# Kernel optimization log

Measured on AMD Instinct MI355X. Metric: run time of the kernel, lower is better.

## Reference

```python
import jax, jax.numpy as jnp
import numpy as np

NUM_GROUPS = 32
EPS = 1e-6


def group_norm(x, gamma, beta):
    # x: [B, C, H, W]; GroupNorm over (channels-in-group, H, W)
    B, C, H, W = x.shape
    xg = x.reshape(B, NUM_GROUPS, C // NUM_GROUPS, H, W)
    mean = xg.mean(axis=(2, 3, 4), keepdims=True)
    var = xg.var(axis=(2, 3, 4), keepdims=True)
    xn = ((xg - mean) * jax.lax.rsqrt(var + EPS)).reshape(B, C, H, W)
    return xn * gamma[None, :, None, None] + beta[None, :, None, None]


def conv1x1(x, w, b):
    # 1x1 conv == channel-mixing matmul. w: [C_out, C_in]
    return jnp.einsum('bchw,oc->bohw', x, w) + b[None, :, None, None]


def setup_inputs() -> dict:
    key = jax.random.key(0)
    ks = jax.random.split(key, 6)
    B, C, H, W = 8, 256, 64, 64
    s = 1.0 / np.sqrt(C)  # fan-in scaled weights (like Conv2d default)
    inp = {
        'x': jax.random.normal(ks[0], (B, C, H, W), jnp.float32),
        'gamma': jnp.ones((C,), jnp.float32),
        'beta': jnp.zeros((C,), jnp.float32),
        'wq': jax.random.normal(ks[1], (C, C), jnp.float32) * s,
        'bq': jnp.zeros((C,), jnp.float32),
        'wk': jax.random.normal(ks[2], (C, C), jnp.float32) * s,
        'bk': jnp.zeros((C,), jnp.float32),
        'wv': jax.random.normal(ks[3], (C, C), jnp.float32) * s,
        'bv': jnp.zeros((C,), jnp.float32),
        'wo': jax.random.normal(ks[4], (C, C), jnp.float32) * s,
        'bo': jnp.zeros((C,), jnp.float32),
    }
    return inp


def reference(x, gamma, beta, wq, bq, wk, bk, wv, bv, wo, bo):
    B, C, H, W = x.shape
    h = group_norm(x, gamma, beta)
    q = conv1x1(h, wq, bq)
    k = conv1x1(h, wk, bk)
    v = conv1x1(h, wv, bv)
    # elu + 1 feature map (nonnegative kernel features)
    q = jax.nn.elu(q) + 1.0
    k = jax.nn.elu(k) + 1.0
    N = H * W
    kf = k.reshape(B, C, N)            # [B, C, N]
    vf = v.reshape(B, C, N)            # [B, C, N]
    qf = q.reshape(B, C, N)            # [B, C, N]
    # kv = k @ v^T : [B, C, C]
    kv = jnp.einsum('bcn,bdn->bcd', kf, vf)
    # h_out[b, n, d] = sum_c q[b, c, n] * kv[b, c, d]; stored channel-first
    h_out = jnp.einsum('bcn,bcd->bdn', qf, kv).reshape(B, C, H, W)
    return x + conv1x1(h_out, wo, bo)
```

## Files before the change

kernel.cpp:

```cpp
#include <hip/hip_runtime.h>
#include <math.h>

#define C_DIM 256
#define N_DIM 4096
#define B_DIM 8

typedef __attribute__((ext_vector_type(8))) short bf16x8;
typedef __attribute__((ext_vector_type(4))) float f32x4;
typedef __attribute__((ext_vector_type(8))) unsigned short us8;
typedef __attribute__((ext_vector_type(4))) unsigned short us4;

__device__ inline unsigned short f2bf(float f) {
    unsigned int u = __float_as_uint(f);
    u += 0x7fffu + ((u >> 16) & 1u);
    return (unsigned short)(u >> 16);
}

__device__ inline void gload_lds16(const void* g, void* l) {
    __builtin_amdgcn_global_load_lds(
        (const __attribute__((address_space(1))) unsigned int*)g,
        (__attribute__((address_space(3))) unsigned int*)l, 16, 0, 0);
}

__global__ __launch_bounds__(256) void prep_kernel(
    const float* __restrict__ wq, const float* __restrict__ wk,
    const float* __restrict__ wv, const float* __restrict__ wo,
    const float* __restrict__ bk, const float* __restrict__ bv,
    const float* __restrict__ x,
    unsigned short* __restrict__ wqb, unsigned short* __restrict__ wkvb,
    unsigned short* __restrict__ wob, float* __restrict__ bkv,
    float2* __restrict__ sums)
{
    int z = blockIdx.x;
    int t = threadIdx.x;
    if (z < 256) {
        const float* s; unsigned short* d;
        int which = z >> 6;
        if (which == 0)      { s = wq; d = wqb; }
        else if (which == 1) { s = wk; d = wkvb; }
        else if (which == 2) { s = wv; d = wkvb + 65536; }
        else                 { s = wo; d = wob; }
        int idx = (z & 63) * 1024 + t * 4;
        float4 v = *(const float4*)(s + idx);
        us4 r; r[0] = f2bf(v.x); r[1] = f2bf(v.y); r[2] = f2bf(v.z); r[3] = f2bf(v.w);
        *(us4*)(d + idx) = r;
    } else if (z == 256) {
        bkv[t]       = bk[t];
        bkv[t + 256] = bv[t];
    } else {
        int bc = z - 257;
        const float* xc = x + (size_t)bc * N_DIM;
        float s = 0.f, q = 0.f;
        for (int i = t; i < 1024; i += 256) {
            float4 v = ((const float4*)xc)[i];
            s += v.x + v.y + v.z + v.w;
            q += v.x*v.x + v.y*v.y + v.z*v.z + v.w*v.w;
        }
        #pragma unroll
        for (int off = 32; off > 0; off >>= 1) {
            s += __shfl_down(s, off);
            q += __shfl_down(q, off);
        }
        __shared__ float red[8];
        int w = t >> 6;
        if ((t & 63) == 0) { red[w*2] = s; red[w*2+1] = q; }
        __syncthreads();
        if (t == 0) {
            sums[bc] = make_float2(red[0]+red[2]+red[4]+red[6],
                                   red[1]+red[3]+red[5]+red[7]);
        }
    }
}

__global__ __launch_bounds__(256) void gn_apply(const float* __restrict__ x,
                                                const float2* __restrict__ sums,
                                                const float* __restrict__ gamma,
                                                const float* __restrict__ beta,
                                                unsigned short* __restrict__ hT) {
    int b = blockIdx.y, n0 = blockIdx.x * 64;
    int t = threadIdx.x;
    __shared__ float scale[256], shift[256];
    __shared__ unsigned short trans[64][264];

    {
        int c = t;
        int gbase = c & ~7;
        float s = 0.f, q = 0.f;
        #pragma unroll
        for (int j = 0; j < 8; j++) {
            float2 u = sums[b*256 + gbase + j];
            s += u.x; q += u.y;
        }
        float mean = s * (1.f/32768.f);
        float var  = q * (1.f/32768.f) - mean*mean;
        float inv  = rsqrtf(var + 1e-6f);
        float gm = gamma[c] * inv;
        scale[c] = gm;
        shift[c] = beta[c] - mean * gm;
    }
    __syncthreads();

    #pragma unroll
    for (int it = 0; it < 16; it++) {
        int c  = it*16 + (t >> 4);
        int nl = (t & 15) * 4;
        float4 v = *(const float4*)(x + ((size_t)(b*C_DIM + c))*N_DIM + n0 + nl);
        float sc = scale[c], sh = shift[c];
        trans[nl+0][c] = f2bf(v.x*sc + sh);
        trans[nl+1][c] = f2bf(v.y*sc + sh);
        trans[nl+2][c] = f2bf(v.z*sc + sh);
        trans[nl+3][c] = f2bf(v.w*sc + sh);
    }
    __syncthreads();

    #pragma unroll
    for (int it = 0; it < 8; it++) {
        int nl = it*8 + (t >> 5);
        int cb = (t & 31) * 8;
        us8 vv = *(us8*)&trans[nl][cb];
        *(us8*)(hT + ((size_t)b*N_DIM + n0 + nl)*C_DIM + cb) = vv;
    }
}

__global__ __launch_bounds__(256) void kvred(const float* __restrict__ src, unsigned short* __restrict__ dst) {
    int gi = (blockIdx.x * 256 + threadIdx.x) * 4;
    int b = gi >> 16, idx = gi & 65535;
    float4 a = make_float4(0.f,0.f,0.f,0.f);
    #pragma unroll
    for (int sp = 0; sp < 16; sp++) {
        float4 v = *(const float4*)(src + (((size_t)b*16 + sp) << 16) + idx);
        a.x += v.x; a.y += v.y; a.z += v.z; a.w += v.w;
    }
    us4 r; r[0] = f2bf(a.x); r[1] = f2bf(a.y); r[2] = f2bf(a.z); r[3] = f2bf(a.w);
    *(us4*)(dst + ((size_t)b << 16) + idx) = r;
}

template<int MODE>
__device__ __forceinline__ void gemm_body(
    const unsigned short* __restrict__ Ab, const unsigned short* __restrict__ Bb,
    const float* __restrict__ bias, const float* __restrict__ residb,
    void* __restrict__ Cb,
    int N, int K, int k0, int Ks, int m_blk, int n_blk, bool elu,
    char* smem)
{
    unsigned short* As = (unsigned short*)smem;
    unsigned short* Bs = As + 4096;

    int t = threadIdx.x;
    int w = t >> 6, l = t & 63;
    int wm = w >> 1, wn = w & 1;
    int l15 = l & 15, quad = l >> 4;

    int srow = w * 16 + (l >> 2);
    int skc  = (l & 3) * 8;

    f32x4 acc[4][4];
    #pragma unroll
    for (int i = 0; i < 4; i++)
        #pragma unroll
        for (int j = 0; j < 4; j++)
            #pragma unroll
            for (int r = 0; r < 4; r++) acc[i][j][r] = 0.f;

    const unsigned short* Asw = As + (wm*64 + l15)*32 + quad*8;
    const unsigned short* Bsw = Bs + (wn*64 + l15)*32 + quad*8;
    unsigned short* Asl = As + w*512 + l*8;
    unsigned short* Bsl = Bs + w*512 + l*8;

    for (int kt = k0; kt < k0 + Ks; kt += 32) {
        #pragma unroll
        for (int rep = 0; rep < 2; rep++) {
            gload_lds16(Ab + (size_t)(m_blk + rep*64 + srow) * K + kt + skc, Asl + rep*2048);
            gload_lds16(Bb + (size_t)(n_blk + rep*64 + srow) * K + kt + skc, Bsl + rep*2048);
        }
        __syncthreads();
        bf16x8 af[4], bfr[4];
        #pragma unroll
        for (int i = 0; i < 4; i++) af[i]  = *(const bf16x8*)(Asw + i*16*32);
        #pragma unroll
        for (int j = 0; j < 4; j++) bfr[j] = *(const bf16x8*)(Bsw + j*16*32);
        #pragma unroll
        for (int i = 0; i < 4; i++)
            #pragma unroll
            for (int j = 0; j < 4; j++)
                acc[i][j] = __builtin_amdgcn_mfma_f32_16x16x32_bf16(af[i], bfr[j], acc[i][j], 0, 0, 0);
        __syncthreads();
    }

    if (MODE == 0 || MODE == 1 || MODE == 4) {
        unsigned short* ep = (unsigned short*)smem;
        int row0 = wm*64 + quad*4;
        int col0 = wn*64 + l15;
        #pragma unroll
        for (int i = 0; i < 4; i++) {
            #pragma unroll
            for (int j = 0; j < 4; j++) {
                int cl = col0 + j*16;
                #pragma unroll
                for (int r = 0; r < 4; r++) {
                    int rl = row0 + i*16 + r;
                    float val = acc[i][j][r];
                    if (MODE == 0) {
                        val += bias[n_blk + cl];
                        val = val > 0.f ? val + 1.f : __expf(val);
                    } else if (MODE == 1) {
                        val += bias[m_blk + rl];
                        if (elu) val = val > 0.f ? val + 1.f : __expf(val);
                    }
                    ep[rl*136 + cl] = f2bf(val);
                }
            }
        }
        __syncthreads();
        unsigned short* Cp = (unsigned short*)Cb;
        #pragma unroll
        for (int it = 0; it < 8; it++) {
            int row = it*16 + (t >> 4);
            int col = (t & 15) * 8;
            us8 vv = *(us8*)(ep + row*136 + col);
            *(us8*)(Cp + (size_t)(m_blk + row) * N + n_blk + col) = vv;
        }
    } else {
        float* ep32 = (float*)smem;
        float* Cp = (float*)Cb;
        #pragma unroll
        for (int h = 0; h < 2; h++) {
            if (wm == h) {
                int row0 = quad*4;
                int col0 = wn*64 + l15;
                #pragma unroll
                for (int i = 0; i < 4; i++)
                    #pragma unroll
                    for (int j = 0; j < 4; j++)
                        #pragma unroll
                        for (int r = 0; r < 4; r++)
                            ep32[(row0 + i*16 + r)*140 + col0 + j*16] = acc[i][j][r];
            }
            __syncthreads();
            #pragma unroll
            for (int it = 0; it < 8; it++) {
                int rl  = it*8 + (t >> 5);
                int row = m_blk + h*64 + rl;
                int col = (t & 31) * 4;
                f32x4 vv = *(f32x4*)(ep32 + rl*140 + col);
                if (MODE == 5) {
                    float bi = bias[row];
                    float4 rv = *(const float4*)(residb + (size_t)row * N + n_blk + col);
                    vv[0] += bi + rv.x; vv[1] += bi + rv.y;
                    vv[2] += bi + rv.z; vv[3] += bi + rv.w;
                }
                *(f32x4*)(Cp + (size_t)row * N + n_blk + col) = vv;
            }
            __syncthreads();
        }
    }
}

__global__ __launch_bounds__(256) void qkv_kernel(
    const unsigned short* __restrict__ hT, const unsigned short* __restrict__ wqb,
    const unsigned short* __restrict__ wkvb,
    const float* __restrict__ bq, const float* __restrict__ bkv,
    unsigned short* __restrict__ qT, unsigned short* __restrict__ kvbuf)
{
    __shared__ __align__(16) char smem[36864];
    int z = blockIdx.x;
    if (z < 512) {
        int b = z >> 6, rem = z & 63;
        int m_blk = (rem >> 1) * 128, n_blk = (rem & 1) * 128;
        gemm_body<0>(hT + (size_t)b*1048576, wqb, bq, nullptr,
                     qT + (size_t)b*1048576,
                     256, 256, 0, 256, m_blk, n_blk, true, smem);
    } else {
        int iz = z - 512;
        int b = iz >> 7, rem = iz & 127;
        int m_blk = (rem >> 5) * 128, n_blk = (rem & 31) * 128;
        gemm_body<1>(wkvb, hT + (size_t)b*1048576, bkv, nullptr,
                     kvbuf + (size_t)b*2097152,
                     4096, 256, 0, 256, m_blk, n_blk, m_blk < 256, smem);
    }
}

template<int MODE>
__global__ __launch_bounds__(256) void gemm_nt(
    const unsigned short* __restrict__ A, const unsigned short* __restrict__ B,
    const float* __restrict__ bias, const float* __restrict__ resid,
    void* __restrict__ Cout,
    int N, int K, int splits,
    size_t sA, size_t sB, size_t sC, size_t sR, int elem4)
{
    __shared__ __align__(16) char smem[36864];
    int b  = blockIdx.z / splits;
    int sp = blockIdx.z % splits;
    int Ks = K / splits;
    size_t cbase = (MODE == 3) ? ((size_t)(b*splits + sp)) * sC : (size_t)b * sC;
    void* Cb = elem4 ? (void*)((float*)Cout + cbase) : (void*)((unsigned short*)Cout + cbase);
    gemm_body<MODE>(A + b*sA, B + b*sB, bias,
                    resid ? resid + b*sR : nullptr, Cb,
                    N, K, sp*Ks, Ks, blockIdx.y*128, blockIdx.x*128, false, smem);
}

extern "C" void kernel_launch(void* const* d_in, const int* in_sizes, int n_in,
                              void* d_out, int out_size, void* d_ws, size_t ws_size,
                              hipStream_t stream) {
    const float* x     = (const float*)d_in[0];
    const float* gamma = (const float*)d_in[1];
    const float* beta  = (const float*)d_in[2];
    const float* wq    = (const float*)d_in[3];
    const float* bq    = (const float*)d_in[4];
    const float* wk    = (const float*)d_in[5];
    const float* bk    = (const float*)d_in[6];
    const float* wv    = (const float*)d_in[7];
    const float* bv    = (const float*)d_in[8];
    const float* wo    = (const float*)d_in[9];
    const float* bo    = (const float*)d_in[10];
    float* out = (float*)d_out;

    const size_t TEN = (size_t)B_DIM * C_DIM * N_DIM;
    unsigned short* ws16  = (unsigned short*)d_ws;
    unsigned short* hT    = ws16;
    unsigned short* qT    = hT    + TEN;
    unsigned short* kvbuf = qT    + TEN;
    unsigned short* kvb   = kvbuf + 2*TEN;
    unsigned short* M2b   = kvb   + 524288;
    unsigned short* wqb   = M2b   + 524288;
    unsigned short* wkvb  = wqb   + 65536;
    unsigned short* wob   = wkvb  + 131072;
    float*          bkv   = (float*)(wob + 65536);
    float2*         sums  = (float2*)(bkv + 512);
    float*          kvf   = (float*)(sums + 2048);

    prep_kernel<<<dim3(2305), 256, 0, stream>>>(wq, wk, wv, wo, bk, bv, x,
                                                wqb, wkvb, wob, bkv, sums);
    gn_apply<<<dim3(N_DIM/64, B_DIM), 256, 0, stream>>>(x, sums, gamma, beta, hT);
    qkv_kernel<<<dim3(1536), 256, 0, stream>>>(hT, wqb, wkvb, bq, bkv, qT, kvbuf);
    gemm_nt<3><<<dim3(2, 2, B_DIM*16), 256, 0, stream>>>(
        kvbuf, kvbuf + 1048576, nullptr, nullptr, kvf,
        256, 4096, 16, 2097152, 2097152, 65536, 0, 1);
    kvred<<<dim3(512), 256, 0, stream>>>(kvf, kvb);
    gemm_nt<4><<<dim3(2, 2, B_DIM), 256, 0, stream>>>(
        wob, kvb, nullptr, nullptr, M2b,
        256, 256, 1, 0, 65536, 65536, 0, 0);
    gemm_nt<5><<<dim3(32, 2, B_DIM), 256, 0, stream>>>(
        M2b, qT, bo, x, out,
        4096, 256, 1, 65536, 1048576, 1048576, 1048576, 1);
}
```

Before: 185.9 us.

## Double-buffer LDS tiles in GEMM main loop and split bf16 epilogue by halves

The GEMM body now keeps two LDS stages and issues the global-to-LDS loads for the next K tile before running the MFMAs on the current one, so memory latency overlaps with compute. It replaces the two per-iteration __syncthreads with one explicit vmcnt wait plus barrier, and raises wave priority around the MFMA block. The bf16 epilogue is staged in two 64-row halves so the LDS footprint drops to 32KB for those modes, which may allow more blocks per CU. The cost is an extra barrier round in the epilogue and some loss of scheduling freedom from the sched_barriers.

```diff
diff --git a/kernel.cpp b/kernel.cpp
--- a/kernel.cpp
+++ b/kernel.cpp
@@ -143,8 +143,7 @@
     int N, int K, int k0, int Ks, int m_blk, int n_blk, bool elu,
     char* smem)
 {
-    unsigned short* As = (unsigned short*)smem;
-    unsigned short* Bs = As + 4096;
+    unsigned short* lds = (unsigned short*)smem;
 
     int t = threadIdx.x;
     int w = t >> 6, l = t & 63;
@@ -162,63 +161,85 @@
             #pragma unroll
             for (int r = 0; r < 4; r++) acc[i][j][r] = 0.f;
 
-    const unsigned short* Asw = As + (wm*64 + l15)*32 + quad*8;
-    const unsigned short* Bsw = Bs + (wn*64 + l15)*32 + quad*8;
-    unsigned short* Asl = As + w*512 + l*8;
-    unsigned short* Bsl = Bs + w*512 + l*8;
-
-    for (int kt = k0; kt < k0 + Ks; kt += 32) {
+    auto stage = [&](int buf, int kt) {
+        unsigned short* Asl = lds + buf*8192 + t*8;
+        unsigned short* Bsl = Asl + 4096;
         #pragma unroll
         for (int rep = 0; rep < 2; rep++) {
             gload_lds16(Ab + (size_t)(m_blk + rep*64 + srow) * K + kt + skc, Asl + rep*2048);
             gload_lds16(Bb + (size_t)(n_blk + rep*64 + srow) * K + kt + skc, Bsl + rep*2048);
         }
-        __syncthreads();
+    };
+
+    const int nt = Ks >> 5;
+
+    stage(0, k0);
+    __builtin_amdgcn_sched_barrier(0);
+    asm volatile("s_waitcnt vmcnt(0)" ::: "memory");
+    __builtin_amdgcn_s_barrier();
+
+    for (int kt = 0; kt < nt; ++kt) {
+        int cur = kt & 1;
+        if (kt + 1 < nt) stage(cur ^ 1, k0 + (kt + 1) * 32);
+        __builtin_amdgcn_sched_barrier(0);
+
+        const unsigned short* Aw = lds + cur*8192 + (wm*64 + l15)*32 + quad*8;
+        const unsigned short* Bw = lds + cur*8192 + 4096 + (wn*64 + l15)*32 + quad*8;
         bf16x8 af[4], bfr[4];
         #pragma unroll
-        for (int i = 0; i < 4; i++) af[i]  = *(const bf16x8*)(Asw + i*16*32);
-        #pragma unroll
-        for (int j = 0; j < 4; j++) bfr[j] = *(const bf16x8*)(Bsw + j*16*32);
+        for (int i = 0; i < 4; i++) af[i]  = *(const bf16x8*)(Aw + i*512);
+        #pragma unroll
+        for (int j = 0; j < 4; j++) bfr[j] = *(const bf16x8*)(Bw + j*512);
+        __builtin_amdgcn_s_setprio(1);
         #pragma unroll
         for (int i = 0; i < 4; i++)
             #pragma unroll
             for (int j = 0; j < 4; j++)
                 acc[i][j] = __builtin_amdgcn_mfma_f32_16x16x32_bf16(af[i], bfr[j], acc[i][j], 0, 0, 0);
-        __syncthreads();
+        __builtin_amdgcn_s_setprio(0);
+        __builtin_amdgcn_sched_barrier(0);
+        asm volatile("s_waitcnt vmcnt(0)" ::: "memory");
+        __builtin_amdgcn_s_barrier();
     }
 
     if (MODE == 0 || MODE == 1 || MODE == 4) {
         unsigned short* ep = (unsigned short*)smem;
-        int row0 = wm*64 + quad*4;
-        int col0 = wn*64 + l15;
-        #pragma unroll
-        for (int i = 0; i < 4; i++) {
-            #pragma unroll
-            for (int j = 0; j < 4; j++) {
-                int cl = col0 + j*16;
+        unsigned short* Cp = (unsigned short*)Cb;
+        #pragma unroll
+        for (int h = 0; h < 2; h++) {
+            if (wm == h) {
+                int row0 = quad*4;
+                int col0 = wn*64 + l15;
                 #pragma unroll
-                for (int r = 0; r < 4; r++) {
-                    int rl = row0 + i*16 + r;
-                    float val = acc[i][j][r];
-                    if (MODE == 0) {
-                        val += bias[n_blk + cl];
-                        val = val > 0.f ? val + 1.f : __expf(val);
-                    } else if (MODE == 1) {
-                        val += bias[m_blk + rl];
-                        if (elu) val = val > 0.f ? val + 1.f : __expf(val);
+                for (int i = 0; i < 4; i++) {
+                    #pragma unroll
+                    for (int j = 0; j < 4; j++) {
+                        int cl = col0 + j*16;
+                        #pragma unroll
+                        for (int r = 0; r < 4; r++) {
+                            int rl = row0 + i*16 + r;
+                            float val = acc[i][j][r];
+                            if (MODE == 0) {
+                                val += bias[n_blk + cl];
+                                val = val > 0.f ? val + 1.f : __expf(val);
+                            } else if (MODE == 1) {
+                                val += bias[m_blk + h*64 + rl];
+                                if (elu) val = val > 0.f ? val + 1.f : __expf(val);
+                            }
+                            ep[rl*136 + cl] = f2bf(val);
+                        }
                     }
-                    ep[rl*136 + cl] = f2bf(val);
                 }
             }
-        }
-        __syncthreads();
-        unsigned short* Cp = (unsigned short*)Cb;
-        #pragma unroll
-        for (int it = 0; it < 8; it++) {
-            int row = it*16 + (t >> 4);
-            int col = (t & 15) * 8;
-            us8 vv = *(us8*)(ep + row*136 + col);
-            *(us8*)(Cp + (size_t)(m_blk + row) * N + n_blk + col) = vv;
+            __syncthreads();
+            #pragma unroll
+            for (int it = 0; it < 4; it++) {
+                int row = it*16 + (t >> 4);
+                int col = (t & 15) * 8;
+                us8 vv = *(us8*)(ep + row*136 + col);
+                *(us8*)(Cp + (size_t)(m_blk + h*64 + row) * N + n_blk + col) = vv;
+            }
+            __syncthreads();
         }
     } else {
         float* ep32 = (float*)smem;
@@ -262,7 +283,7 @@
     const float* __restrict__ bq, const float* __restrict__ bkv,
     unsigned short* __restrict__ qT, unsigned short* __restrict__ kvbuf)
 {
-    __shared__ __align__(16) char smem[36864];
+    __shared__ __align__(16) char smem[32768];
     int z = blockIdx.x;
     if (z < 512) {
         int b = z >> 6, rem = z & 63;
@@ -288,7 +309,7 @@
     int N, int K, int splits,
     size_t sA, size_t sB, size_t sC, size_t sR, int elem4)
 {
-    __shared__ __align__(16) char smem[36864];
+    __shared__ __align__(16) char smem[(MODE == 3 || MODE == 5) ? 36864 : 32768];
     int b  = blockIdx.z / splits;
     int sp = blockIdx.z % splits;
     int Ks = K / splits;
```

Measured after the change: 191.8 us. 1.03x slower.
